# Optimization experiments

Hardware: AMD Instinct MI355X
Metric: run time of the kernel (lower is better)

## Reference

```python
import jax, jax.numpy as jnp
import numpy as np

V, E, H, B, S = 32000, 512, 1024, 128, 512
NEG = -1e9


def setup_inputs() -> dict:
    key = jax.random.key(0)
    ks = jax.random.split(key, 12)
    s = 0.02
    return {
        "previous_word": jax.random.randint(ks[0], (B, 1), 0, V),
        "h_0": jax.random.normal(ks[1], (B, H), jnp.float32),
        "c_0": jax.random.normal(ks[2], (B, H), jnp.float32),
        "ctx": jax.random.normal(ks[3], (B, S, H), jnp.float32),
        "ctx_mask": jnp.zeros((B, S), dtype=bool),
        "emb": jax.random.normal(ks[4], (V, E), jnp.float32) * s,
        "W_ih": jax.random.normal(ks[5], (4 * H, E), jnp.float32) * s,
        "W_hh": jax.random.normal(ks[6], (4 * H, H), jnp.float32) * s,
        "b_ih": jnp.zeros((4 * H,), jnp.float32),
        "b_hh": jnp.zeros((4 * H,), jnp.float32),
        "W_in": jax.random.normal(ks[7], (H, H), jnp.float32) * s,
        "W_out": jax.random.normal(ks[8], (H, 2 * H), jnp.float32) * s,
        "W_dec": jax.random.normal(ks[9], (V, H), jnp.float32) * s,
        "b_dec": jnp.zeros((V,), jnp.float32),
    }


def reference(previous_word, h_0, c_0, ctx, ctx_mask, emb, W_ih, W_hh, b_ih, b_hh, W_in, W_out, W_dec, b_dec):
    # embedding lookup + squeeze; dropout is identity in eval mode
    x = emb[previous_word[:, 0]]                       # [B, E]
    # LSTMCell: gate order i, f, g, o (PyTorch convention)
    gates = x @ W_ih.T + b_ih + h_0 @ W_hh.T + b_hh    # [B, 4H]
    i, f, g, o = jnp.split(gates, 4, axis=1)
    i = jax.nn.sigmoid(i)
    f = jax.nn.sigmoid(f)
    g = jnp.tanh(g)
    o = jax.nn.sigmoid(o)
    c_1 = f * c_0 + i * g
    h_1 = o * jnp.tanh(c_1)
    # SoftDotAttention
    target = h_1 @ W_in.T                               # [B, H]
    attn = jnp.einsum('bsh,bh->bs', ctx, target)        # [B, S]
    attn = jnp.where(ctx_mask, NEG, attn)
    alpha = jax.nn.softmax(attn, axis=1)
    weighted = jnp.einsum('bs,bsh->bh', alpha, ctx)     # [B, H]
    h_tilde = jnp.tanh(jnp.concatenate([weighted, h_1], axis=1) @ W_out.T)
    logit = h_tilde @ W_dec.T + b_dec                   # [B, V]
    return (h_1, c_1, alpha, logit)
```

## Files before the change

kernel.cpp:

```cpp
#include <hip/hip_runtime.h>
#include <hip/hip_bf16.h>
#include <cstdint>

#define NEG_BIG (-1.0e9f)

typedef __attribute__((ext_vector_type(8))) short short8_t;
typedef __attribute__((ext_vector_type(4))) float f32x4;

typedef __attribute__((address_space(1))) const unsigned int gu32_t;
typedef __attribute__((address_space(3))) unsigned int lu32_t;

__device__ __forceinline__ short f2bf(float x) {
  union { float f; unsigned u; } v; v.f = x;
  unsigned r = v.u + 0x7fffu + ((v.u >> 16) & 1u);
  return (short)(r >> 16);
}
__device__ __forceinline__ float sigmoidf_(float x) { return 1.0f / (1.0f + __expf(-x)); }

__device__ __forceinline__ void lds_barrier() {
  asm volatile("s_waitcnt lgkmcnt(0)\n\ts_barrier" ::: "memory");
}
__device__ __forceinline__ void block_barrier() {
  asm volatile("" ::: "memory");
  __builtin_amdgcn_s_barrier();
  asm volatile("" ::: "memory");
}

__launch_bounds__(256, 2)
__global__ void k_ggemm(const int* __restrict__ prev, const float* __restrict__ emb,
                        const float* __restrict__ h0,
                        const float* __restrict__ W_ih, const float* __restrict__ W_hh,
                        const float* __restrict__ b_ih, const float* __restrict__ b_hh,
                        float* __restrict__ gates) {
  __shared__ __align__(16) short lA[2][128 * 64];
  __shared__ __align__(16) short lW[2][16 * 64];
  const int tid = threadIdx.x;
  const int wid = tid >> 6, l = tid & 63, l15 = l & 15, khalf = l >> 4;
  const int nblk = blockIdx.x;

  const int arow = tid >> 1, apart = tid & 1;
  const int aswz = (arow & 7) << 4;
  const float* embrow = emb + (size_t)prev[arow] * 512;
  const float* h0row = h0 + (size_t)arow * 1024;

  const int wn = (tid * 4) >> 6;
  const int wkq = (tid * 4) & 63;
  const float* wih = W_ih + (size_t)(nblk * 16 + wn) * 512;
  const float* whh = W_hh + (size_t)(nblk * 16 + wn) * 1024;

  f32x4 acc[2];
  acc[0] = (f32x4){0.f, 0.f, 0.f, 0.f};
  acc[1] = (f32x4){0.f, 0.f, 0.f, 0.f};

  float4 aF[8], wR;
  auto stage_regs = [&](int k0) {
    const int col0 = k0 + apart * 32;
    const float* asrc = (col0 < 512) ? (embrow + col0) : (h0row + (col0 - 512));
#pragma unroll
    for (int q = 0; q < 8; ++q) aF[q] = *(const float4*)(asrc + q * 4);
    const int kg = k0 + wkq;
    wR = (kg < 512) ? *(const float4*)(wih + kg) : *(const float4*)(whh + (kg - 512));
  };
  auto write_lds = [&](int buf) {
    char* drow = (char*)lA[buf] + arow * 128;
#pragma unroll
    for (int q = 0; q < 4; ++q) {
      short8_t s;
      s[0] = f2bf(aF[2 * q].x); s[1] = f2bf(aF[2 * q].y);
      s[2] = f2bf(aF[2 * q].z); s[3] = f2bf(aF[2 * q].w);
      s[4] = f2bf(aF[2 * q + 1].x); s[5] = f2bf(aF[2 * q + 1].y);
      s[6] = f2bf(aF[2 * q + 1].z); s[7] = f2bf(aF[2 * q + 1].w);
      *(short8_t*)(drow + ((apart * 64 + q * 16) ^ aswz)) = s;
    }
    short4 h4;
    h4.x = f2bf(wR.x); h4.y = f2bf(wR.y); h4.z = f2bf(wR.z); h4.w = f2bf(wR.w);
    *(short4*)((char*)lW[buf] + wn * 128 + ((wkq * 2) ^ ((wn & 7) << 4))) = h4;
  };
  auto compute = [&](int buf) {
#pragma unroll
    for (int ks = 0; ks < 2; ++ks) {
      const int ubyte = ks * 64 + khalf * 16;
      short8_t bfrag = *(const short8_t*)((char*)lW[buf] + l15 * 128 + (ubyte ^ ((l15 & 7) << 4)));
#pragma unroll
      for (int r = 0; r < 2; ++r) {
        const int mrow = wid * 32 + r * 16 + l15;
        short8_t afrag = *(const short8_t*)((char*)lA[buf] + mrow * 128 + (ubyte ^ ((mrow & 7) << 4)));
        acc[r] = __builtin_amdgcn_mfma_f32_16x16x32_bf16(afrag, bfrag, acc[r], 0, 0, 0);
      }
    }
  };

  stage_regs(0);
  write_lds(0);
  for (int t = 0; t < 24; ++t) {
    const int cur = t & 1;
    if (t + 1 < 24) stage_regs((t + 1) << 6);
    lds_barrier();
    compute(cur);
    if (t + 1 < 24) write_lds(cur ^ 1);
  }

  const int n = nblk * 16 + l15;
  const float bias = b_ih[n] + b_hh[n];
#pragma unroll
  for (int r = 0; r < 2; ++r) {
    int mb = wid * 32 + r * 16 + khalf * 4;
#pragma unroll
    for (int e = 0; e < 4; ++e)
      gates[(size_t)(mb + e) * 4096 + n] = acc[r][e] + bias;
  }
}

template <int MB, int WN, int EPI>
__launch_bounds__(256, 2)
__global__ void k_gemm(const short* __restrict__ A, int lda,
                       const float* __restrict__ Wa, int ldwa, int Ka,
                       const float* __restrict__ Wb, int ldwb, int Ktot,
                       const float* __restrict__ bias0, const float* __restrict__ bias1,
                       float* __restrict__ outF, short* __restrict__ outB, int ldo,
                       int kstride, size_t pstride) {
  constexpr int BN = WN * 16;
  constexpr int MREP = (MB == 128) ? 2 * WN : 1;
  constexpr int AU = MB / 32;
  constexpr int WLOADS = (BN * 64) / 1024;
  __shared__ __align__(16) short lA[2][MB * 64];
  __shared__ __align__(16) short lW[2][BN * 64];
  const int kc = blockIdx.z;
  A += (size_t)kc * kstride;
  Wa += (size_t)kc * kstride;
  if (outF) outF += (size_t)kc * pstride;
  const int tid = threadIdx.x;
  const int wid = tid >> 6, l = tid & 63, l15 = l & 15, khalf = l >> 4;
  const int nblk = blockIdx.x;
  const int mrow0 = blockIdx.y * MB;
  const int m_wave = (WN == 1) ? wid * (MB / 4) : 0;
  const int nb_local = (WN == 4) ? wid * 16 : 0;

  const int arow = (MB == 128) ? (tid >> 1) : (tid >> 2);
  const int apart = (MB == 128) ? (tid & 1) : (tid & 3);
  const int abase = apart * (AU * 16);
  const int aswz = (arow & 7) << 4;
  const short* Arow = A + (size_t)(mrow0 + arow) * lda + apart * (AU * 8);

  int wn_[WLOADS], wkq_[WLOADS];
#pragma unroll
  for (int j = 0; j < WLOADS; ++j) {
    int idx = j * 1024 + tid * 4;
    wn_[j] = idx >> 6;
    wkq_[j] = idx & 63;
  }

  f32x4 acc[MREP];
#pragma unroll
  for (int r = 0; r < MREP; ++r) acc[r] = (f32x4){0.f, 0.f, 0.f, 0.f};

  short8_t aR[AU];
  float4 wR[WLOADS];

  auto stage_regs = [&](int k0) {
#pragma unroll
    for (int q = 0; q < AU; ++q) aR[q] = *(const short8_t*)(Arow + k0 + q * 8);
#pragma unroll
    for (int j = 0; j < WLOADS; ++j) {
      int kg = k0 + wkq_[j];
      const float* p = (kg < Ka) ? (Wa + (size_t)(nblk * BN + wn_[j]) * ldwa + kg)
                                 : (Wb + (size_t)(nblk * BN + wn_[j]) * ldwb + (kg - Ka));
      wR[j] = *(const float4*)p;
    }
  };
  auto write_lds = [&](int buf) {
    char* drow = (char*)lA[buf] + arow * 128;
#pragma unroll
    for (int q = 0; q < AU; ++q)
      *(short8_t*)(drow + ((abase + q * 16) ^ aswz)) = aR[q];
#pragma unroll
    for (int j = 0; j < WLOADS; ++j) {
      short4 h4;
      h4.x = f2bf(wR[j].x); h4.y = f2bf(wR[j].y); h4.z = f2bf(wR[j].z); h4.w = f2bf(wR[j].w);
      *(short4*)((char*)lW[buf] + wn_[j] * 128 + ((wkq_[j] * 2) ^ ((wn_[j] & 7) << 4))) = h4;
    }
  };
  auto compute = [&](int buf) {
#pragma unroll
    for (int ks = 0; ks < 2; ++ks) {
      const int ubyte = ks * 64 + khalf * 16;
      const int nrow = nb_local + l15;
      short8_t bfrag = *(const short8_t*)((char*)lW[buf] + nrow * 128 + (ubyte ^ ((nrow & 7) << 4)));
#pragma unroll
      for (int r = 0; r < MREP; ++r) {
        const int mrow = m_wave + r * 16 + l15;
        short8_t afrag = *(const short8_t*)((char*)lA[buf] + mrow * 128 + (ubyte ^ ((mrow & 7) << 4)));
        acc[r] = __builtin_amdgcn_mfma_f32_16x16x32_bf16(afrag, bfrag, acc[r], 0, 0, 0);
      }
    }
  };

  const int NT = Ktot >> 6;
  stage_regs(0);
  write_lds(0);
  for (int t = 0; t < NT; ++t) {
    const int cur = t & 1;
    if (t + 1 < NT) stage_regs((t + 1) << 6);
    lds_barrier();
    compute(cur);
    if (t + 1 < NT) write_lds(cur ^ 1);
  }

  const int n = nblk * BN + nb_local + l15;
  float bias = 0.f;
  if (bias0) bias = bias0[n];
  if (bias1) bias += bias1[n];
#pragma unroll
  for (int r = 0; r < MREP; ++r) {
    int mb = mrow0 + m_wave + r * 16 + khalf * 4;
#pragma unroll
    for (int e = 0; e < 4; ++e) {
      float v = acc[r][e] + bias;
      if (EPI == 1) {
        outB[(size_t)(mb + e) * ldo + n] = f2bf(tanhf(v));
      } else {
        outF[(size_t)(mb + e) * ldo + n] = v;
      }
    }
  }
}

__global__ void k_lstm(const float* __restrict__ gates, const float* __restrict__ c0,
                       float* __restrict__ h1_out, float* __restrict__ c1_out,
                       short* __restrict__ A3) {
  int t = blockIdx.x * 256 + threadIdx.x;
  int b = t >> 10, h = t & 1023;
  const float* g = gates + (size_t)b * 4096;
  float ig = sigmoidf_(g[h]);
  float fg = sigmoidf_(g[1024 + h]);
  float gg = tanhf(g[2048 + h]);
  float og = sigmoidf_(g[3072 + h]);
  float c1 = fg * c0[t] + ig * gg;
  float h1 = og * tanhf(c1);
  c1_out[t] = c1;
  h1_out[t] = h1;
  A3[(size_t)b * 2048 + 1024 + h] = f2bf(h1);
}

__launch_bounds__(256, 2)
__global__ void k_attn(const float* __restrict__ ctx, const float* __restrict__ tp,
                       const unsigned char* __restrict__ mask,
                       float* __restrict__ scores, float* __restrict__ part) {
  __shared__ __align__(16) float lds[2][8 * 1024];
  __shared__ float sml[8];
  const int b = blockIdx.x >> 2, chunk = blockIdx.x & 3;
  const int tid = threadIdx.x;
  const int wid = tid >> 6, l = tid & 63;
  float4 t4[4], w4[4];
#pragma unroll
  for (int j = 0; j < 4; ++j) {
    float4 a = {0.f, 0.f, 0.f, 0.f};
#pragma unroll
    for (int p = 0; p < 4; ++p) {
      const float4 v = *(const float4*)(tp + (size_t)p * 131072 + (size_t)b * 1024 + j * 256 + l * 4);
      a.x += v.x; a.y += v.y; a.z += v.z; a.w += v.w;
    }
    t4[j] = a;
    w4[j].x = 0.f; w4[j].y = 0.f; w4[j].z = 0.f; w4[j].w = 0.f;
  }
  float m = -INFINITY, lsum = 0.f;
  const int s0 = chunk * 128;
  const float* cb = ctx + ((size_t)b * 512 + s0) * 1024;
  const unsigned char* mk = mask + (size_t)b * 512 + s0;

  auto stage = [&](int buf, int tt) {
    const char* src = (const char*)(cb + (size_t)tt * 8192);
    char* dst = (char*)&lds[buf][0];
#pragma unroll
    for (int i = 0; i < 8; ++i) {
      const int off = i * 4096 + tid * 16;
      __builtin_amdgcn_global_load_lds((gu32_t*)(src + off), (lu32_t*)(dst + off), 16, 0, 0);
    }
  };

  stage(0, 0);
  int buf = 0;
  for (int t = 0; t < 16; ++t) {
    if (t < 15) {
      stage(buf ^ 1, t + 1);
      asm volatile("s_waitcnt vmcnt(8)" ::: "memory");
    } else {
      asm volatile("s_waitcnt vmcnt(0)" ::: "memory");
    }
    block_barrier();
#pragma unroll
    for (int rr = 0; rr < 2; ++rr) {
      const int r = wid * 2 + rr;
      const float* row = &lds[buf][r * 1024];
      float4 c0 = *(const float4*)(row + l * 4);
      float4 c1 = *(const float4*)(row + 256 + l * 4);
      float4 c2 = *(const float4*)(row + 512 + l * 4);
      float4 c3 = *(const float4*)(row + 768 + l * 4);
      float p = c0.x * t4[0].x + c0.y * t4[0].y + c0.z * t4[0].z + c0.w * t4[0].w +
                c1.x * t4[1].x + c1.y * t4[1].y + c1.z * t4[1].z + c1.w * t4[1].w +
                c2.x * t4[2].x + c2.y * t4[2].y + c2.z * t4[2].z + c2.w * t4[2].w +
                c3.x * t4[3].x + c3.y * t4[3].y + c3.z * t4[3].z + c3.w * t4[3].w;
#pragma unroll
      for (int off = 32; off > 0; off >>= 1) p += __shfl_xor(p, off);
      const int sg = t * 8 + r;
      if (mk[sg]) p = NEG_BIG;
      if (l == 0) scores[(size_t)b * 512 + s0 + sg] = p;
      float mn = fmaxf(m, p);
      float scale = __expf(m - mn);
      float e = __expf(p - mn);
      lsum = lsum * scale + e;
      w4[0].x = w4[0].x * scale + e * c0.x; w4[0].y = w4[0].y * scale + e * c0.y;
      w4[0].z = w4[0].z * scale + e * c0.z; w4[0].w = w4[0].w * scale + e * c0.w;
      w4[1].x = w4[1].x * scale + e * c1.x; w4[1].y = w4[1].y * scale + e * c1.y;
      w4[1].z = w4[1].z * scale + e * c1.z; w4[1].w = w4[1].w * scale + e * c1.w;
      w4[2].x = w4[2].x * scale + e * c2.x; w4[2].y = w4[2].y * scale + e * c2.y;
      w4[2].z = w4[2].z * scale + e * c2.z; w4[2].w = w4[2].w * scale + e * c2.w;
      w4[3].x = w4[3].x * scale + e * c3.x; w4[3].y = w4[3].y * scale + e * c3.y;
      w4[3].z = w4[3].z * scale + e * c3.z; w4[3].w = w4[3].w * scale + e * c3.w;
      m = mn;
    }
    block_barrier();
    buf ^= 1;
  }

  float* cbuf = &lds[0][0];
#pragma unroll
  for (int j = 0; j < 4; ++j) *(float4*)(cbuf + wid * 1024 + j * 256 + l * 4) = w4[j];
  if (l == 0) { sml[wid] = m; sml[4 + wid] = lsum; }
  __syncthreads();
  const float M = fmaxf(fmaxf(sml[0], sml[1]), fmaxf(sml[2], sml[3]));
  const float sc0 = __expf(sml[0] - M), sc1 = __expf(sml[1] - M);
  const float sc2 = __expf(sml[2] - M), sc3 = __expf(sml[3] - M);
  const float L = sml[4] * sc0 + sml[5] * sc1 + sml[6] * sc2 + sml[7] * sc3;
  const float4 v0 = *(const float4*)(cbuf + 0 * 1024 + tid * 4);
  const float4 v1 = *(const float4*)(cbuf + 1 * 1024 + tid * 4);
  const float4 v2 = *(const float4*)(cbuf + 2 * 1024 + tid * 4);
  const float4 v3 = *(const float4*)(cbuf + 3 * 1024 + tid * 4);
  float4 o;
  o.x = v0.x * sc0 + v1.x * sc1 + v2.x * sc2 + v3.x * sc3;
  o.y = v0.y * sc0 + v1.y * sc1 + v2.y * sc2 + v3.y * sc3;
  o.z = v0.z * sc0 + v1.z * sc1 + v2.z * sc2 + v3.z * sc3;
  o.w = v0.w * sc0 + v1.w * sc1 + v2.w * sc2 + v3.w * sc3;
  float* pp = part + ((size_t)b * 4 + chunk) * 1028;
  *(float4*)(pp + tid * 4) = o;
  if (tid == 0) { pp[1024] = M; pp[1025] = L; }
}

__launch_bounds__(256, 4)
__global__ void k_finish(const float* __restrict__ scores, const float* __restrict__ part,
                         float* __restrict__ alpha, short* __restrict__ A3) {
  __shared__ float sm[4], sl[4];
  int b = blockIdx.x, t = threadIdx.x;
  if (t < 4) {
    sm[t] = part[((size_t)b * 4 + t) * 1028 + 1024];
    sl[t] = part[((size_t)b * 4 + t) * 1028 + 1025];
  }
  __syncthreads();
  float M = fmaxf(fmaxf(sm[0], sm[1]), fmaxf(sm[2], sm[3]));
  float scl[4];
  float L = 0.f;
#pragma unroll
  for (int i = 0; i < 4; ++i) {
    scl[i] = __expf(sm[i] - M);
    L += sl[i] * scl[i];
  }
  float inv = 1.0f / L;
  float s0 = scores[(size_t)b * 512 + t];
  float s1 = scores[(size_t)b * 512 + 256 + t];
  alpha[(size_t)b * 512 + t] = __expf(s0 - M) * inv;
  alpha[(size_t)b * 512 + 256 + t] = __expf(s1 - M) * inv;
  float ax = 0.f, ay = 0.f, az = 0.f, aw = 0.f;
#pragma unroll
  for (int i = 0; i < 4; ++i) {
    const float4 w = *(const float4*)(part + ((size_t)b * 4 + i) * 1028 + t * 4);
    ax += scl[i] * w.x; ay += scl[i] * w.y; az += scl[i] * w.z; aw += scl[i] * w.w;
  }
  short4 o4;
  o4.x = f2bf(ax * inv); o4.y = f2bf(ay * inv); o4.z = f2bf(az * inv); o4.w = f2bf(aw * inv);
  *(short4*)(A3 + (size_t)b * 2048 + t * 4) = o4;
}

__global__ void k_htilde(const float* __restrict__ wp, short* __restrict__ ht) {
  int t = blockIdx.x * 256 + threadIdx.x;
  float s = 0.f;
#pragma unroll
  for (int p = 0; p < 8; ++p) s += wp[(size_t)p * 131072 + t];
  ht[t] = f2bf(tanhf(s));
}

extern "C" void kernel_launch(void* const* d_in, const int* in_sizes, int n_in,
                              void* d_out, int out_size, void* d_ws, size_t ws_size,
                              hipStream_t stream) {
  const int* prev = (const int*)d_in[0];
  const float* h0 = (const float*)d_in[1];
  const float* c0 = (const float*)d_in[2];
  const float* ctx = (const float*)d_in[3];
  const unsigned char* mask = (const unsigned char*)d_in[4];
  const float* emb = (const float*)d_in[5];
  const float* W_ih = (const float*)d_in[6];
  const float* W_hh = (const float*)d_in[7];
  const float* b_ih = (const float*)d_in[8];
  const float* b_hh = (const float*)d_in[9];
  const float* W_in = (const float*)d_in[10];
  const float* W_out = (const float*)d_in[11];
  const float* W_dec = (const float*)d_in[12];
  const float* b_dec = (const float*)d_in[13];

  float* out_h1 = (float*)d_out;
  float* out_c1 = out_h1 + 128 * 1024;
  float* out_alpha = out_c1 + 128 * 1024;
  float* out_logit = out_alpha + 128 * 512;

  char* ws = (char*)d_ws;
  short* A3 = (short*)(ws + 0x000000);
  float* scores = (float*)(ws + 0x100000);
  float* tp = (float*)(ws + 0x200000);
  float* part = (float*)(ws + 0x400000);
  float* wp = (float*)(ws + 0xD00000);
  float* gates = (float*)(ws + 0x1100000);
  short* htilde = (short*)(ws + 0x1400000);

  k_ggemm<<<256, 256, 0, stream>>>(prev, emb, h0, W_ih, W_hh, b_ih, b_hh, gates);
  k_lstm<<<512, 256, 0, stream>>>(gates, c0, out_h1, out_c1, A3);
  k_gemm<128, 1, 0><<<dim3(64, 1, 4), 256, 0, stream>>>(
      A3 + 1024, 2048, W_in, 1024, 1 << 30, W_in, 1024, 256, nullptr, nullptr, tp, nullptr,
      1024, 256, (size_t)131072);
  k_attn<<<512, 256, 0, stream>>>(ctx, tp, mask, scores, part);
  k_finish<<<128, 256, 0, stream>>>(scores, part, out_alpha, A3);
  k_gemm<128, 1, 0><<<dim3(64, 1, 8), 256, 0, stream>>>(
      A3, 2048, W_out, 2048, 1 << 30, W_out, 2048, 256, nullptr, nullptr, wp, nullptr,
      1024, 256, (size_t)131072);
  k_htilde<<<512, 256, 0, stream>>>(wp, htilde);
  k_gemm<128, 4, 0><<<dim3(500, 1, 1), 256, 0, stream>>>(
      htilde, 1024, W_dec, 1024, 1024, W_dec, 1024, 1024, b_dec, nullptr, out_logit, nullptr,
      32000, 0, 0);
}
```

Measured before the change: 143.5 us.

## Split-K the LSTM gate GEMM four ways and reduce partials in the cell kernel

The gate GEMM now runs on a 256x4 grid. Each z-slice covers 384 of the 1536 K columns and writes unbiased partial gate sums to a workspace buffer. The LSTM cell kernel sums the four partials, adds both biases, then applies the gate nonlinearities. The aim is to raise block count and shorten each block's serial K loop on a latency-bound small GEMM. The cost is extra global traffic for the partial buffers. Workspace offsets are repacked to fit the larger partial buffer.

```diff
diff --git a/kernel.cpp b/kernel.cpp
--- a/kernel.cpp
+++ b/kernel.cpp
@@ -27,24 +27,23 @@
 }
 
 __launch_bounds__(256, 2)
-__global__ void k_ggemm(const int* __restrict__ prev, const float* __restrict__ emb,
-                        const float* __restrict__ h0,
-                        const float* __restrict__ W_ih, const float* __restrict__ W_hh,
-                        const float* __restrict__ b_ih, const float* __restrict__ b_hh,
-                        float* __restrict__ gates) {
+__global__ void k_ggemm2(const int* __restrict__ prev, const float* __restrict__ emb,
+                         const float* __restrict__ h0,
+                         const float* __restrict__ W_ih, const float* __restrict__ W_hh,
+                         float* __restrict__ gp) {
   __shared__ __align__(16) short lA[2][128 * 64];
   __shared__ __align__(16) short lW[2][16 * 64];
+  const int kc = blockIdx.z, nblk = blockIdx.x;
   const int tid = threadIdx.x;
   const int wid = tid >> 6, l = tid & 63, l15 = l & 15, khalf = l >> 4;
-  const int nblk = blockIdx.x;
+  const int kbase = kc * 384;
 
   const int arow = tid >> 1, apart = tid & 1;
   const int aswz = (arow & 7) << 4;
   const float* embrow = emb + (size_t)prev[arow] * 512;
   const float* h0row = h0 + (size_t)arow * 1024;
 
-  const int wn = (tid * 4) >> 6;
-  const int wkq = (tid * 4) & 63;
+  const int wn = (tid * 4) >> 6, wkq = (tid * 4) & 63;
   const float* wih = W_ih + (size_t)(nblk * 16 + wn) * 512;
   const float* whh = W_hh + (size_t)(nblk * 16 + wn) * 1024;
 
@@ -54,11 +53,11 @@
 
   float4 aF[8], wR;
   auto stage_regs = [&](int k0) {
-    const int col0 = k0 + apart * 32;
+    const int col0 = kbase + k0 + apart * 32;
     const float* asrc = (col0 < 512) ? (embrow + col0) : (h0row + (col0 - 512));
 #pragma unroll
     for (int q = 0; q < 8; ++q) aF[q] = *(const float4*)(asrc + q * 4);
-    const int kg = k0 + wkq;
+    const int kg = kbase + k0 + wkq;
     wR = (kg < 512) ? *(const float4*)(wih + kg) : *(const float4*)(whh + (kg - 512));
   };
   auto write_lds = [&](int buf) {
@@ -92,23 +91,45 @@
 
   stage_regs(0);
   write_lds(0);
-  for (int t = 0; t < 24; ++t) {
+  for (int t = 0; t < 6; ++t) {
     const int cur = t & 1;
-    if (t + 1 < 24) stage_regs((t + 1) << 6);
+    if (t + 1 < 6) stage_regs((t + 1) << 6);
     lds_barrier();
     compute(cur);
-    if (t + 1 < 24) write_lds(cur ^ 1);
+    if (t + 1 < 6) write_lds(cur ^ 1);
   }
 
   const int n = nblk * 16 + l15;
-  const float bias = b_ih[n] + b_hh[n];
+  float* out = gp + (size_t)kc * 524288;
 #pragma unroll
   for (int r = 0; r < 2; ++r) {
     int mb = wid * 32 + r * 16 + khalf * 4;
 #pragma unroll
     for (int e = 0; e < 4; ++e)
-      gates[(size_t)(mb + e) * 4096 + n] = acc[r][e] + bias;
-  }
+      out[(size_t)(mb + e) * 4096 + n] = acc[r][e];
+  }
+}
+
+__global__ void k_lstm2(const float* __restrict__ gp, const float* __restrict__ b_ih,
+                        const float* __restrict__ b_hh, const float* __restrict__ c0,
+                        float* __restrict__ h1_out, float* __restrict__ c1_out,
+                        short* __restrict__ A3) {
+  int t = blockIdx.x * 256 + threadIdx.x;
+  int b = t >> 10, h = t & 1023;
+  float iv = b_ih[h] + b_hh[h];
+  float fv = b_ih[1024 + h] + b_hh[1024 + h];
+  float gv = b_ih[2048 + h] + b_hh[2048 + h];
+  float ov = b_ih[3072 + h] + b_hh[3072 + h];
+#pragma unroll
+  for (int kc = 0; kc < 4; ++kc) {
+    const float* g = gp + (size_t)kc * 524288 + (size_t)b * 4096;
+    iv += g[h]; fv += g[1024 + h]; gv += g[2048 + h]; ov += g[3072 + h];
+  }
+  float c1 = sigmoidf_(fv) * c0[t] + sigmoidf_(iv) * tanhf(gv);
+  float h1 = sigmoidf_(ov) * tanhf(c1);
+  c1_out[t] = c1;
+  h1_out[t] = h1;
+  A3[(size_t)b * 2048 + 1024 + h] = f2bf(h1);
 }
 
 template <int MB, int WN, int EPI>
@@ -225,23 +246,6 @@
   }
 }
 
-__global__ void k_lstm(const float* __restrict__ gates, const float* __restrict__ c0,
-                       float* __restrict__ h1_out, float* __restrict__ c1_out,
-                       short* __restrict__ A3) {
-  int t = blockIdx.x * 256 + threadIdx.x;
-  int b = t >> 10, h = t & 1023;
-  const float* g = gates + (size_t)b * 4096;
-  float ig = sigmoidf_(g[h]);
-  float fg = sigmoidf_(g[1024 + h]);
-  float gg = tanhf(g[2048 + h]);
-  float og = sigmoidf_(g[3072 + h]);
-  float c1 = fg * c0[t] + ig * gg;
-  float h1 = og * tanhf(c1);
-  c1_out[t] = c1;
-  h1_out[t] = h1;
-  A3[(size_t)b * 2048 + 1024 + h] = f2bf(h1);
-}
-
 __launch_bounds__(256, 2)
 __global__ void k_attn(const float* __restrict__ ctx, const float* __restrict__ tp,
                        const unsigned char* __restrict__ mask,
@@ -416,12 +420,12 @@
   float* scores = (float*)(ws + 0x100000);
   float* tp = (float*)(ws + 0x200000);
   float* part = (float*)(ws + 0x400000);
-  float* wp = (float*)(ws + 0xD00000);
-  float* gates = (float*)(ws + 0x1100000);
-  short* htilde = (short*)(ws + 0x1400000);
-
-  k_ggemm<<<256, 256, 0, stream>>>(prev, emb, h0, W_ih, W_hh, b_ih, b_hh, gates);
-  k_lstm<<<512, 256, 0, stream>>>(gates, c0, out_h1, out_c1, A3);
+  float* wp = (float*)(ws + 0x700000);
+  float* gp = (float*)(ws + 0xB00000);
+  short* htilde = (short*)(ws + 0x1300000);
+
+  k_ggemm2<<<dim3(256, 1, 4), 256, 0, stream>>>(prev, emb, h0, W_ih, W_hh, gp);
+  k_lstm2<<<512, 256, 0, stream>>>(gp, b_ih, b_hh, c0, out_h1, out_c1, A3);
   k_gemm<128, 1, 0><<<dim3(64, 1, 4), 256, 0, stream>>>(
       A3 + 1024, 2048, W_in, 1024, 1 << 30, W_in, 1024, 256, nullptr, nullptr, tp, nullptr,
       1024, 256, (size_t)131072);
```

Result: faster. 139.7 us (-2.6%).
